# Optimization experiments

Hardware: AMD Instinct MI355X
Metric: run time of the kernel (lower is better)

## Reference

```python
import jax, jax.numpy as jnp
import numpy as np

HEADS = 8


def setup_inputs() -> dict:
    key = jax.random.key(0)
    ks = jax.random.split(key, 6)
    B, N, D = 4, 2048, 512
    return {
        "x": jax.random.normal(ks[0], (B, N, D), dtype=jnp.float32),
        "pos": jax.random.uniform(ks[1], (B, N, 3), dtype=jnp.float32),
        "qkv_w": jax.random.normal(ks[2], (3 * D, D), dtype=jnp.float32) * 0.02,
        "qkv_b": jax.random.normal(ks[3], (3 * D,), dtype=jnp.float32) * 0.02,
        "out_w": jax.random.normal(ks[4], (D, D), dtype=jnp.float32) * 0.02,
        "out_b": jax.random.normal(ks[5], (D,), dtype=jnp.float32) * 0.02,
    }


def reference(x, pos, qkv_w, qkv_b, out_w, out_b):
    B, N, D = x.shape
    H = HEADS
    Dh = D // H
    scale = D ** (-0.5)  # NOTE: original uses full dim, not head dim

    # QKV projection -> [3, B, H, N, Dh]
    qkv = (x @ qkv_w.T + qkv_b).reshape(B, N, 3, H, Dh).transpose(2, 0, 3, 1, 4)
    q, k, v = qkv[0], qkv[1], qkv[2]

    # partial 3D RoPE on first 6 head dims (3 axis pairs)
    theta = pos * jnp.pi                    # [B, N, 3]
    sin = jnp.sin(theta)[:, None]           # [B, 1, N, 3] broadcasts over heads
    cos = jnp.cos(theta)[:, None]

    def rotate(t):
        x_rot = t[..., :6]
        x1 = x_rot[..., 0::2]               # [B, H, N, 3]
        x2 = x_rot[..., 1::2]
        return jnp.concatenate(
            [x1 * cos - x2 * sin, x1 * sin + x2 * cos, t[..., 6:]], axis=-1
        )

    q = rotate(q)
    k = rotate(k)

    attn = jax.nn.softmax(jnp.einsum("bhqd,bhkd->bhqk", q, k) * scale, axis=-1)
    out = jnp.einsum("bhqk,bhkd->bhqd", attn, v)          # [B, H, N, Dh]
    out = out.transpose(0, 2, 1, 3).reshape(B, N, D)
    return out @ out_w.T + out_b
```

## Files before the change

kernel.cpp:

```cpp
#include <hip/hip_runtime.h>
#include <stdint.h>

typedef __attribute__((ext_vector_type(4))) float f32x4;
typedef __attribute__((ext_vector_type(16))) float f32x16;
typedef __attribute__((ext_vector_type(8))) short bf16x8;
typedef __attribute__((ext_vector_type(4))) unsigned short u16x4;

__device__ __forceinline__ unsigned short f2bf(float f) {
    unsigned int u = __builtin_bit_cast(unsigned int, f);
    u += 0x7fffu + ((u >> 16) & 1u);
    return (unsigned short)(u >> 16);
}
__device__ __forceinline__ float fexp2(float x) {
#if __has_builtin(__builtin_amdgcn_exp2f)
    return __builtin_amdgcn_exp2f(x);
#else
    return exp2f(x);
#endif
}
__device__ __forceinline__ unsigned int cvt_pk_bf16(float lo, float hi) {
    unsigned int r;
    asm("v_cvt_pk_bf16_f32 %0, %1, %2" : "=v"(r) : "v"(lo), "v"(hi));
    return r;
}

__global__ void k_cvt2(const float* __restrict__ w1,
                       const float* __restrict__ w2,
                       unsigned short* __restrict__ out) {
    const int C2 = 196608;
    int i = blockIdx.x * blockDim.x + threadIdx.x;
    f32x4 v;
    if (i < C2) v = ((const f32x4*)w1)[i];
    else        v = ((const f32x4*)w2)[i - C2];
    u16x4 o;
    o.x = f2bf(v.x); o.y = f2bf(v.y); o.z = f2bf(v.z); o.w = f2bf(v.w);
    ((u16x4*)out)[i] = o;
}

__global__ __launch_bounds__(256, 3)
void k_gemm_qkv(const float* __restrict__ Xf,
                const unsigned short* __restrict__ Bm,
                const float* __restrict__ bias,
                const float* __restrict__ pos,
                unsigned short* __restrict__ Qb,
                unsigned short* __restrict__ Kb,
                unsigned short* __restrict__ VT) {
    const float PI = 3.14159265358979323846f;
    const float QS = 0.04419417382415922f * 1.44269504088896341f;
    const int K = 512;
    __shared__ float Asf[2][128 * 32];
    __shared__ unsigned short Bs[2][128 * 32];
    const int tid = threadIdx.x;
    const int lane = tid & 63;
    const int w = tid >> 6;
    const int wr = (w >> 1) * 64, wc = (w & 1) * 64;
    const int g = lane >> 4, fr = lane & 15;

    const int bid = blockIdx.x;
    const int xcd = bid & 7, loc = bid >> 3;
    const int rowb = xcd * 8 + (loc & 7);
    const int colb = loc >> 3;

    f32x4 acc[4][4];
#pragma unroll
    for (int i = 0; i < 4; ++i)
#pragma unroll
        for (int j = 0; j < 4; ++j) acc[i][j] = f32x4{0.f, 0.f, 0.f, 0.f};

    const int srow8 = lane >> 3;
    const int scaf = ((lane & 7) ^ srow8) * 4;
    const int srow16 = lane >> 2;
    const int schunk = ((lane & 3) ^ (srow16 & 3)) * 8;
    const unsigned short* Bseg0 = Bm + (size_t)(colb * 128 + w * 16 + srow16) * K + schunk;
    const unsigned short* Bseg1 = Bm + (size_t)(colb * 128 + (w + 4) * 16 + srow16) * K + schunk;

    auto stage = [&](int bsel, int k0) {
        char* la = (char*)&Asf[bsel][0];
        char* lb = (char*)&Bs[bsel][0];
#pragma unroll
        for (int i = 0; i < 4; ++i) {
            const float* src = Xf + (size_t)(rowb * 128 + (w + 4 * i) * 8 + srow8) * 512 + scaf + k0;
            __builtin_amdgcn_global_load_lds((const __attribute__((address_space(1))) void*)src,
                                             (__attribute__((address_space(3))) void*)(la + (w + 4 * i) * 1024), 16, 0, 0);
        }
        __builtin_amdgcn_global_load_lds((const __attribute__((address_space(1))) void*)(Bseg0 + k0),
                                         (__attribute__((address_space(3))) void*)(lb + w * 1024), 16, 0, 0);
        __builtin_amdgcn_global_load_lds((const __attribute__((address_space(1))) void*)(Bseg1 + k0),
                                         (__attribute__((address_space(3))) void*)(lb + (w + 4) * 1024), 16, 0, 0);
    };
    auto compute = [&](int bsel) {
        bf16x8 af[4], bfv[4];
        const int rcb = (g ^ (fr & 3)) * 8;
        const int pa0 = ((2 * g) ^ (fr & 7)) * 4;
        const int pa1 = ((2 * g + 1) ^ (fr & 7)) * 4;
#pragma unroll
        for (int mi = 0; mi < 4; ++mi) {
            int row = wr + mi * 16 + fr;
            f32x4 lo = *(const f32x4*)&Asf[bsel][row * 32 + pa0];
            f32x4 hi = *(const f32x4*)&Asf[bsel][row * 32 + pa1];
            union { unsigned int u[4]; bf16x8 v; } c;
            c.u[0] = cvt_pk_bf16(lo.x, lo.y);
            c.u[1] = cvt_pk_bf16(lo.z, lo.w);
            c.u[2] = cvt_pk_bf16(hi.x, hi.y);
            c.u[3] = cvt_pk_bf16(hi.z, hi.w);
            af[mi] = c.v;
        }
#pragma unroll
        for (int ni = 0; ni < 4; ++ni)
            bfv[ni] = *(const bf16x8*)&Bs[bsel][(wc + ni * 16 + fr) * 32 + rcb];
        __builtin_amdgcn_s_setprio(1);
#pragma unroll
        for (int mi = 0; mi < 4; ++mi)
#pragma unroll
            for (int ni = 0; ni < 4; ++ni)
                acc[mi][ni] = __builtin_amdgcn_mfma_f32_16x16x32_bf16(af[mi], bfv[ni], acc[mi][ni], 0, 0, 0);
        __builtin_amdgcn_s_setprio(0);
    };

    const int nt = K >> 5;
    stage(0, 0);
    asm volatile("s_waitcnt vmcnt(0)" ::: "memory");
    __builtin_amdgcn_s_barrier();
    int cur = 0;
#pragma unroll 1
    for (int t = 0; t < nt; ++t) {
        if (t < nt - 1) stage(cur ^ 1, (t + 1) << 5);
        compute(cur);
        if (t < nt - 1) {
            asm volatile("s_waitcnt vmcnt(0)" ::: "memory");
            __builtin_amdgcn_s_barrier();
        }
        cur ^= 1;
    }

    const int jrot = (fr < 3) ? fr : ((fr < 6) ? fr - 3 : 0);
    const int shbase = lane & 48;
#pragma unroll
    for (int mi = 0; mi < 4; ++mi) {
#pragma unroll
        for (int ni = 0; ni < 4; ++ni) {
            int row = rowb * 128 + wr + mi * 16 + g * 4;
            int col = colb * 128 + wc + ni * 16 + fr;
            float bz = bias[col];
            float v[4];
#pragma unroll
            for (int r = 0; r < 4; ++r) v[r] = acc[mi][ni][r] + bz;
            int b = row >> 11, n = row & 2047;
            if (colb < 8) {
                const int isQ = (colb < 4);
                int qcol = isQ ? col : col - 512;
                int h = qcol >> 6, dh = qcol & 63;
                if (ni == 0) {
#pragma unroll
                    for (int r = 0; r < 4; ++r) {
                        float x1 = __shfl(v[r], shbase + 2 * jrot, 64);
                        float x2 = __shfl(v[r], shbase + 2 * jrot + 1, 64);
                        if (fr < 6) {
                            float th = pos[(row + r) * 3 + jrot] * PI;
                            float sn = __sinf(th), cs = __cosf(th);
                            v[r] = (fr < 3) ? (x1 * cs - x2 * sn) : (x1 * sn + x2 * cs);
                        }
                    }
                }
                float qs = isQ ? QS : 1.f;
                unsigned short* dst = isQ ? Qb : Kb;
                size_t rb = (size_t)(b * 8 + h) * 2048 + n;
#pragma unroll
                for (int r = 0; r < 4; ++r)
                    dst[(rb + r) * 64 + dh] = f2bf(v[r] * qs);
            } else {
                int vcol = col - 1024;
                int h = vcol >> 6, dh = vcol & 63;
                int q2 = (n >> 2) & 3;
                int np = n + (q2 == 1 ? 4 : (q2 == 2 ? -4 : 0));
                u16x4 o;
#pragma unroll
                for (int r = 0; r < 4; ++r) o[r] = f2bf(v[r]);
                *(u16x4*)&VT[((size_t)(b * 8 + h) * 64 + dh) * 2048 + np] = o;
            }
        }
    }
}

__global__ __launch_bounds__(256, 4)
void k_gemm_out(const unsigned short* __restrict__ A,
                const unsigned short* __restrict__ Bm,
                const float* __restrict__ bias,
                float* __restrict__ Cout) {
    const int K = 512, N = 512;
    __shared__ unsigned short As[2][128 * 32];
    __shared__ unsigned short Bs[2][64 * 32];
    const int tid = threadIdx.x;
    const int lane = tid & 63;
    const int w = tid >> 6;
    const int wr = (w >> 1) * 64, wc = (w & 1) * 32;
    const int g = lane >> 4, fr = lane & 15;

    const int bid = blockIdx.x;
    const int xcd = bid & 7, loc = bid >> 3;
    const int rowb = xcd * 8 + (loc & 7);
    const int colb = loc >> 3;

    f32x4 acc[4][2];
#pragma unroll
    for (int i = 0; i < 4; ++i)
#pragma unroll
        for (int j = 0; j < 2; ++j) acc[i][j] = f32x4{0.f, 0.f, 0.f, 0.f};

    const int srow16 = lane >> 2;
    const int schunk = ((lane & 3) ^ (srow16 & 3)) * 8;
    const unsigned short* Aseg0 = A + (size_t)(rowb * 128 + w * 16 + srow16) * K + schunk;
    const unsigned short* Aseg1 = A + (size_t)(rowb * 128 + (w + 4) * 16 + srow16) * K + schunk;
    const unsigned short* Bseg  = Bm + (size_t)(colb * 64 + w * 16 + srow16) * K + schunk;

    auto stage = [&](int bsel, int k0) {
        char* la = (char*)&As[bsel][0];
        char* lb = (char*)&Bs[bsel][0];
        __builtin_amdgcn_global_load_lds((const __attribute__((address_space(1))) void*)(Aseg0 + k0),
                                         (__attribute__((address_space(3))) void*)(la + w * 1024), 16, 0, 0);
        __builtin_amdgcn_global_load_lds((const __attribute__((address_space(1))) void*)(Aseg1 + k0),
                                         (__attribute__((address_space(3))) void*)(la + (w + 4) * 1024), 16, 0, 0);
        __builtin_amdgcn_global_load_lds((const __attribute__((address_space(1))) void*)(Bseg + k0),
                                         (__attribute__((address_space(3))) void*)(lb + w * 1024), 16, 0, 0);
    };
    auto compute = [&](int bsel) {
        bf16x8 af[4], bfv[2];
        const int rc = (g ^ (fr & 3)) * 8;
#pragma unroll
        for (int mi = 0; mi < 4; ++mi)
            af[mi] = *(const bf16x8*)&As[bsel][(wr + mi * 16 + fr) * 32 + rc];
#pragma unroll
        for (int ni = 0; ni < 2; ++ni)
            bfv[ni] = *(const bf16x8*)&Bs[bsel][(wc + ni * 16 + fr) * 32 + rc];
        __builtin_amdgcn_s_setprio(1);
#pragma unroll
        for (int mi = 0; mi < 4; ++mi)
#pragma unroll
            for (int ni = 0; ni < 2; ++ni)
                acc[mi][ni] = __builtin_amdgcn_mfma_f32_16x16x32_bf16(af[mi], bfv[ni], acc[mi][ni], 0, 0, 0);
        __builtin_amdgcn_s_setprio(0);
    };

    const int nt = K >> 5;
    stage(0, 0);
    asm volatile("s_waitcnt vmcnt(0)" ::: "memory");
    __builtin_amdgcn_s_barrier();
    int cur = 0;
#pragma unroll 1
    for (int t = 0; t < nt; ++t) {
        if (t < nt - 1) stage(cur ^ 1, (t + 1) << 5);
        compute(cur);
        if (t < nt - 1) {
            asm volatile("s_waitcnt vmcnt(0)" ::: "memory");
            __builtin_amdgcn_s_barrier();
        }
        cur ^= 1;
    }

#pragma unroll
    for (int mi = 0; mi < 4; ++mi) {
#pragma unroll
        for (int ni = 0; ni < 2; ++ni) {
            int row = rowb * 128 + wr + mi * 16 + g * 4;
            int col = colb * 64 + wc + ni * 16 + fr;
            float bz = bias[col];
#pragma unroll
            for (int r = 0; r < 4; ++r)
                Cout[(size_t)(row + r) * N + col] = acc[mi][ni][r] + bz;
        }
    }
}

__global__ __launch_bounds__(512, 2)
void k_attn(const unsigned short* __restrict__ Qb,
            const unsigned short* __restrict__ Kb,
            const unsigned short* __restrict__ VT,
            unsigned short* __restrict__ Ob) {
    __shared__ unsigned short smem[2][2][2][4096];
    const int tid = threadIdx.x, lane = tid & 63, w = tid >> 6;
    const int wl = w & 3, half = w >> 2;
    const int l31 = lane & 31, hi = lane >> 5;
    const int bid = blockIdx.x;
    const int loc = bid >> 3;
    const int bh = (bid & 7) * 4 + (loc >> 3);
    const int qb = loc & 7;
    const int b = bh >> 3, h = bh & 7;
    const int qr0 = qb * 256 + wl * 64;
    const unsigned short* Q = Qb + (size_t)bh * 2048 * 64;
    const unsigned short* K = Kb + (size_t)bh * 2048 * 64;
    const unsigned short* V = VT + (size_t)bh * 64 * 2048;
    const int thalf = half * 16;

    const int srow8 = lane >> 3;
    const int swc = ((lane & 7) ^ srow8) << 3;
    const int sA = wl, sB = wl + 4;

    bf16x8 bq0[4], bq1[4];
#pragma unroll
    for (int ds = 0; ds < 4; ++ds) {
        bq0[ds] = *(const bf16x8*)&Q[(size_t)(qr0 + l31) * 64 + ds * 16 + hi * 8];
        bq1[ds] = *(const bf16x8*)&Q[(size_t)(qr0 + 32 + l31) * 64 + ds * 16 + hi * 8];
    }

    f32x16 oT00, oT01, oT10, oT11;
#pragma unroll
    for (int i = 0; i < 16; ++i) { oT00[i] = 0.f; oT01[i] = 0.f; oT10[i] = 0.f; oT11[i] = 0.f; }
    float lp0 = 0.f, lp1 = 0.f;

    auto stage = [&](int bsel, int t) {
        const int kv0 = t * 64;
        const unsigned short* k0 = K + (size_t)(kv0 + sA * 8 + srow8) * 64 + swc;
        const unsigned short* k1 = K + (size_t)(kv0 + sB * 8 + srow8) * 64 + swc;
        const unsigned short* v0 = V + (size_t)(sA * 8 + srow8) * 2048 + kv0 + swc;
        const unsigned short* v1 = V + (size_t)(sB * 8 + srow8) * 2048 + kv0 + swc;
        char* dk = (char*)&smem[half][0][bsel][0];
        char* dv = (char*)&smem[half][1][bsel][0];
        __builtin_amdgcn_global_load_lds((const __attribute__((address_space(1))) void*)k0,
                                         (__attribute__((address_space(3))) void*)(dk + sA * 1024), 16, 0, 0);
        __builtin_amdgcn_global_load_lds((const __attribute__((address_space(1))) void*)k1,
                                         (__attribute__((address_space(3))) void*)(dk + sB * 1024), 16, 0, 0);
        __builtin_amdgcn_global_load_lds((const __attribute__((address_space(1))) void*)v0,
                                         (__attribute__((address_space(3))) void*)(dv + sA * 1024), 16, 0, 0);
        __builtin_amdgcn_global_load_lds((const __attribute__((address_space(1))) void*)v1,
                                         (__attribute__((address_space(3))) void*)(dv + sB * 1024), 16, 0, 0);
    };

    auto pack8 = [&](const float* p) -> bf16x8 {
        union { unsigned int u[4]; bf16x8 v; } c;
        c.u[0] = cvt_pk_bf16(p[0], p[1]);
        c.u[1] = cvt_pk_bf16(p[2], p[3]);
        c.u[2] = cvt_pk_bf16(p[4], p[5]);
        c.u[3] = cvt_pk_bf16(p[6], p[7]);
        return c.v;
    };

    auto compute = [&](int bsel) {
        const unsigned short* KsC = &smem[half][0][bsel][0];
        const unsigned short* VtC = &smem[half][1][bsel][0];
        bf16x8 pb0[4], pb1[4];
        {
            f32x16 s0, s1;
#pragma unroll
            for (int i = 0; i < 16; ++i) { s0[i] = 0.f; s1[i] = 0.f; }
            __builtin_amdgcn_s_setprio(1);
#pragma unroll
            for (int ds = 0; ds < 4; ++ds) {
                const int c = ((((ds << 1) | hi) ^ (l31 & 7)) << 3);
                bf16x8 ka0 = *(const bf16x8*)&KsC[l31 * 64 + c];
                bf16x8 ka1 = *(const bf16x8*)&KsC[(32 + l31) * 64 + c];
                s0 = __builtin_amdgcn_mfma_f32_32x32x16_bf16(ka0, bq0[ds], s0, 0, 0, 0);
                s1 = __builtin_amdgcn_mfma_f32_32x32x16_bf16(ka1, bq0[ds], s1, 0, 0, 0);
            }
            __builtin_amdgcn_s_setprio(0);
            float p0[16], p1[16], lsum = 0.f;
#pragma unroll
            for (int r = 0; r < 16; ++r) {
                p0[r] = fexp2(s0[r]);
                p1[r] = fexp2(s1[r]);
                lsum += p0[r] + p1[r];
            }
            lp0 += lsum;
            pb0[0] = pack8(p0); pb0[1] = pack8(p0 + 8);
            pb0[2] = pack8(p1); pb0[3] = pack8(p1 + 8);
        }
        {
            f32x16 s0, s1;
#pragma unroll
            for (int i = 0; i < 16; ++i) { s0[i] = 0.f; s1[i] = 0.f; }
            __builtin_amdgcn_s_setprio(1);
#pragma unroll
            for (int ds = 0; ds < 4; ++ds) {
                const int c = ((((ds << 1) | hi) ^ (l31 & 7)) << 3);
                bf16x8 ka0 = *(const bf16x8*)&KsC[l31 * 64 + c];
                bf16x8 ka1 = *(const bf16x8*)&KsC[(32 + l31) * 64 + c];
                s0 = __builtin_amdgcn_mfma_f32_32x32x16_bf16(ka0, bq1[ds], s0, 0, 0, 0);
                s1 = __builtin_amdgcn_mfma_f32_32x32x16_bf16(ka1, bq1[ds], s1, 0, 0, 0);
            }
            __builtin_amdgcn_s_setprio(0);
            __builtin_amdgcn_s_setprio(1);
#pragma unroll
            for (int kb = 0; kb < 4; ++kb) {
                const int c = ((((kb << 1) | hi) ^ (l31 & 7)) << 3);
                bf16x8 av0 = *(const bf16x8*)&VtC[l31 * 64 + c];
                bf16x8 av1 = *(const bf16x8*)&VtC[(32 + l31) * 64 + c];
                oT00 = __builtin_amdgcn_mfma_f32_32x32x16_bf16(av0, pb0[kb], oT00, 0, 0, 0);
                oT01 = __builtin_amdgcn_mfma_f32_32x32x16_bf16(av1, pb0[kb], oT01, 0, 0, 0);
            }
            __builtin_amdgcn_s_setprio(0);
            float p0[16], p1[16], lsum = 0.f;
#pragma unroll
            for (int r = 0; r < 16; ++r) {
                p0[r] = fexp2(s0[r]);
                p1[r] = fexp2(s1[r]);
                lsum += p0[r] + p1[r];
            }
            lp1 += lsum;
            pb1[0] = pack8(p0); pb1[1] = pack8(p0 + 8);
            pb1[2] = pack8(p1); pb1[3] = pack8(p1 + 8);
        }
        __builtin_amdgcn_s_setprio(1);
#pragma unroll
        for (int kb = 0; kb < 4; ++kb) {
            const int c = ((((kb << 1) | hi) ^ (l31 & 7)) << 3);
            bf16x8 av0 = *(const bf16x8*)&VtC[l31 * 64 + c];
            bf16x8 av1 = *(const bf16x8*)&VtC[(32 + l31) * 64 + c];
            oT10 = __builtin_amdgcn_mfma_f32_32x32x16_bf16(av0, pb1[kb], oT10, 0, 0, 0);
            oT11 = __builtin_amdgcn_mfma_f32_32x32x16_bf16(av1, pb1[kb], oT11, 0, 0, 0);
        }
        __builtin_amdgcn_s_setprio(0);
    };

    stage(0, thalf);
    asm volatile("s_waitcnt vmcnt(0)" ::: "memory");
    __builtin_amdgcn_s_barrier();
    int cur = 0;
#pragma unroll 1
    for (int t = 0; t < 16; ++t) {
        if (t < 15) stage(cur ^ 1, thalf + t + 1);
        compute(cur);
        if (t < 15) {
            asm volatile("s_waitcnt vmcnt(0)" ::: "memory");
            __builtin_amdgcn_s_barrier();
        }
        cur ^= 1;
    }

    float* mrg = (float*)&smem[0][0][0][0];
    float* slot = mrg + (size_t)(wl * 64 + lane) * 33;
#pragma unroll 1
    for (int st = 0; st < 2; ++st) {
        f32x16& a0 = st ? oT10 : oT00;
        f32x16& a1 = st ? oT11 : oT01;
        float lp = st ? lp1 : lp0;
        __syncthreads();
        if (half) {
#pragma unroll
            for (int i = 0; i < 16; ++i) { slot[i] = a0[i]; slot[16 + i] = a1[i]; }
            slot[32] = lp;
        }
        __syncthreads();
        if (!half) {
            float lf = lp + slot[32];
            lf += __shfl_xor(lf, 32, 64);
            float il = 1.f / lf;
            size_t rowbase = (size_t)(b * 2048 + qr0 + st * 32 + l31) * 512 + h * 64;
#pragma unroll
            for (int grp = 0; grp < 4; ++grp) {
                u16x4 o0, o1;
#pragma unroll
                for (int i = 0; i < 4; ++i) {
                    o0[i] = f2bf((a0[grp * 4 + i] + slot[grp * 4 + i]) * il);
                    o1[i] = f2bf((a1[grp * 4 + i] + slot[16 + grp * 4 + i]) * il);
                }
                int dv0 = grp * 8 + 4 * hi;
                *(u16x4*)&Ob[rowbase + dv0] = o0;
                *(u16x4*)&Ob[rowbase + 32 + dv0] = o1;
            }
        }
    }
}

extern "C" void kernel_launch(void* const* d_in, const int* in_sizes, int n_in,
                              void* d_out, int out_size, void* d_ws, size_t ws_size,
                              hipStream_t stream) {
    const float* x     = (const float*)d_in[0];
    const float* pos   = (const float*)d_in[1];
    const float* qkv_w = (const float*)d_in[2];
    const float* qkv_b = (const float*)d_in[3];
    const float* out_w = (const float*)d_in[4];
    const float* out_b = (const float*)d_in[5];
    float* out = (float*)d_out;

    unsigned short* W1b = (unsigned short*)d_ws;
    unsigned short* W2b = W1b + (size_t)1536 * 512;
    unsigned short* Qb  = W2b + (size_t)512 * 512;
    unsigned short* Kb  = Qb  + (size_t)4194304;
    unsigned short* VTb = Kb  + (size_t)4194304;
    unsigned short* Ob  = VTb + (size_t)4194304;

    k_cvt2<<<1024, 256, 0, stream>>>(qkv_w, out_w, W1b);
    k_gemm_qkv<<<768, 256, 0, stream>>>(x, W1b, qkv_b, pos, Qb, Kb, VTb);
    k_attn<<<256, 512, 0, stream>>>(Qb, Kb, VTb, Ob);
    k_gemm_out<<<512, 256, 0, stream>>>(Ob, W2b, out_b, out);
}
```

Measured before the change: 83.96 us.

## Software-pipeline attention loop: defer PV by one tile with triple-buffered LDS

New measurement: 86.30 us. 1.03x slower.

```diff
diff --git a/kernel.cpp b/kernel.cpp
--- a/kernel.cpp
+++ b/kernel.cpp
@@ -276,7 +276,7 @@
             const unsigned short* __restrict__ Kb,
             const unsigned short* __restrict__ VT,
             unsigned short* __restrict__ Ob) {
-    __shared__ unsigned short smem[2][2][2][4096];
+    __shared__ unsigned short smem[2][2][3][4096];
     const int tid = threadIdx.x, lane = tid & 63, w = tid >> 6;
     const int wl = w & 3, half = w >> 2;
     const int l31 = lane & 31, hi = lane >> 5;
@@ -306,6 +306,7 @@
 #pragma unroll
     for (int i = 0; i < 16; ++i) { oT00[i] = 0.f; oT01[i] = 0.f; oT10[i] = 0.f; oT11[i] = 0.f; }
     float lp0 = 0.f, lp1 = 0.f;
+    bf16x8 pbp0[4], pbp1[4];
 
     auto stage = [&](int bsel, int t) {
         const int kv0 = t * 64;
@@ -334,95 +335,65 @@
         return c.v;
     };
 
-    auto compute = [&](int bsel) {
-        const unsigned short* KsC = &smem[half][0][bsel][0];
-        const unsigned short* VtC = &smem[half][1][bsel][0];
-        bf16x8 pb0[4], pb1[4];
-        {
-            f32x16 s0, s1;
-#pragma unroll
-            for (int i = 0; i < 16; ++i) { s0[i] = 0.f; s1[i] = 0.f; }
-            __builtin_amdgcn_s_setprio(1);
-#pragma unroll
-            for (int ds = 0; ds < 4; ++ds) {
-                const int c = ((((ds << 1) | hi) ^ (l31 & 7)) << 3);
-                bf16x8 ka0 = *(const bf16x8*)&KsC[l31 * 64 + c];
-                bf16x8 ka1 = *(const bf16x8*)&KsC[(32 + l31) * 64 + c];
-                s0 = __builtin_amdgcn_mfma_f32_32x32x16_bf16(ka0, bq0[ds], s0, 0, 0, 0);
-                s1 = __builtin_amdgcn_mfma_f32_32x32x16_bf16(ka1, bq0[ds], s1, 0, 0, 0);
-            }
-            __builtin_amdgcn_s_setprio(0);
-            float p0[16], p1[16], lsum = 0.f;
-#pragma unroll
-            for (int r = 0; r < 16; ++r) {
-                p0[r] = fexp2(s0[r]);
-                p1[r] = fexp2(s1[r]);
-                lsum += p0[r] + p1[r];
-            }
-            lp0 += lsum;
-            pb0[0] = pack8(p0); pb0[1] = pack8(p0 + 8);
-            pb0[2] = pack8(p1); pb0[3] = pack8(p1 + 8);
-        }
-        {
-            f32x16 s0, s1;
-#pragma unroll
-            for (int i = 0; i < 16; ++i) { s0[i] = 0.f; s1[i] = 0.f; }
-            __builtin_amdgcn_s_setprio(1);
-#pragma unroll
-            for (int ds = 0; ds < 4; ++ds) {
-                const int c = ((((ds << 1) | hi) ^ (l31 & 7)) << 3);
-                bf16x8 ka0 = *(const bf16x8*)&KsC[l31 * 64 + c];
-                bf16x8 ka1 = *(const bf16x8*)&KsC[(32 + l31) * 64 + c];
-                s0 = __builtin_amdgcn_mfma_f32_32x32x16_bf16(ka0, bq1[ds], s0, 0, 0, 0);
-                s1 = __builtin_amdgcn_mfma_f32_32x32x16_bf16(ka1, bq1[ds], s1, 0, 0, 0);
-            }
-            __builtin_amdgcn_s_setprio(0);
-            __builtin_amdgcn_s_setprio(1);
-#pragma unroll
-            for (int kb = 0; kb < 4; ++kb) {
-                const int c = ((((kb << 1) | hi) ^ (l31 & 7)) << 3);
-                bf16x8 av0 = *(const bf16x8*)&VtC[l31 * 64 + c];
-                bf16x8 av1 = *(const bf16x8*)&VtC[(32 + l31) * 64 + c];
-                oT00 = __builtin_amdgcn_mfma_f32_32x32x16_bf16(av0, pb0[kb], oT00, 0, 0, 0);
-                oT01 = __builtin_amdgcn_mfma_f32_32x32x16_bf16(av1, pb0[kb], oT01, 0, 0, 0);
-            }
-            __builtin_amdgcn_s_setprio(0);
-            float p0[16], p1[16], lsum = 0.f;
-#pragma unroll
-            for (int r = 0; r < 16; ++r) {
-                p0[r] = fexp2(s0[r]);
-                p1[r] = fexp2(s1[r]);
-                lsum += p0[r] + p1[r];
-            }
-            lp1 += lsum;
-            pb1[0] = pack8(p0); pb1[1] = pack8(p0 + 8);
-            pb1[2] = pack8(p1); pb1[3] = pack8(p1 + 8);
-        }
+    auto qk = [&](const unsigned short* KsC, bf16x8 (&bq)[4], f32x16& s0, f32x16& s1) {
+#pragma unroll
+        for (int i = 0; i < 16; ++i) { s0[i] = 0.f; s1[i] = 0.f; }
+        __builtin_amdgcn_s_setprio(1);
+#pragma unroll
+        for (int ds = 0; ds < 4; ++ds) {
+            const int c = ((((ds << 1) | hi) ^ (l31 & 7)) << 3);
+            bf16x8 ka0 = *(const bf16x8*)&KsC[l31 * 64 + c];
+            bf16x8 ka1 = *(const bf16x8*)&KsC[(32 + l31) * 64 + c];
+            s0 = __builtin_amdgcn_mfma_f32_32x32x16_bf16(ka0, bq[ds], s0, 0, 0, 0);
+            s1 = __builtin_amdgcn_mfma_f32_32x32x16_bf16(ka1, bq[ds], s1, 0, 0, 0);
+        }
+        __builtin_amdgcn_s_setprio(0);
+    };
+    auto pv = [&](const unsigned short* VtC, bf16x8 (&pb)[4], f32x16& o0, f32x16& o1) {
         __builtin_amdgcn_s_setprio(1);
 #pragma unroll
         for (int kb = 0; kb < 4; ++kb) {
             const int c = ((((kb << 1) | hi) ^ (l31 & 7)) << 3);
             bf16x8 av0 = *(const bf16x8*)&VtC[l31 * 64 + c];
             bf16x8 av1 = *(const bf16x8*)&VtC[(32 + l31) * 64 + c];
-            oT10 = __builtin_amdgcn_mfma_f32_32x32x16_bf16(av0, pb1[kb], oT10, 0, 0, 0);
-            oT11 = __builtin_amdgcn_mfma_f32_32x32x16_bf16(av1, pb1[kb], oT11, 0, 0, 0);
+            o0 = __builtin_amdgcn_mfma_f32_32x32x16_bf16(av0, pb[kb], o0, 0, 0, 0);
+            o1 = __builtin_amdgcn_mfma_f32_32x32x16_bf16(av1, pb[kb], o1, 0, 0, 0);
         }
         __builtin_amdgcn_s_setprio(0);
     };
+    auto softmax = [&](f32x16& s0, f32x16& s1, bf16x8 (&pb)[4], float& lp) {
+        float p0[16], p1[16], lsum = 0.f;
+#pragma unroll
+        for (int r = 0; r < 16; ++r) {
+            p0[r] = fexp2(s0[r]);
+            p1[r] = fexp2(s1[r]);
+            lsum += p0[r] + p1[r];
+        }
+        lp += lsum;
+        pb[0] = pack8(p0); pb[1] = pack8(p0 + 8);
+        pb[2] = pack8(p1); pb[3] = pack8(p1 + 8);
+    };
 
     stage(0, thalf);
-    asm volatile("s_waitcnt vmcnt(0)" ::: "memory");
-    __builtin_amdgcn_s_barrier();
-    int cur = 0;
 #pragma unroll 1
     for (int t = 0; t < 16; ++t) {
-        if (t < 15) stage(cur ^ 1, thalf + t + 1);
-        compute(cur);
-        if (t < 15) {
-            asm volatile("s_waitcnt vmcnt(0)" ::: "memory");
-            __builtin_amdgcn_s_barrier();
-        }
-        cur ^= 1;
+        asm volatile("s_waitcnt vmcnt(0)" ::: "memory");
+        __builtin_amdgcn_s_barrier();
+        if (t < 15) stage((t + 1) % 3, thalf + t + 1);
+        const unsigned short* KsC = &smem[half][0][t % 3][0];
+        const unsigned short* VtP = &smem[half][1][(t + 2) % 3][0];
+        f32x16 sA0, sA1, sB0, sB1;
+        qk(KsC, bq0, sA0, sA1);
+        if (t > 0) pv(VtP, pbp0, oT00, oT01);
+        softmax(sA0, sA1, pbp0, lp0);
+        qk(KsC, bq1, sB0, sB1);
+        if (t > 0) pv(VtP, pbp1, oT10, oT11);
+        softmax(sB0, sB1, pbp1, lp1);
+    }
+    {
+        const unsigned short* VtF = &smem[half][1][0][0];
+        pv(VtF, pbp0, oT00, oT01);
+        pv(VtF, pbp1, oT10, oT11);
     }
 
     float* mrg = (float*)&smem[0][0][0][0];
```
